# Performance work log

Measured on AMD Instinct MI355X. Metric: run time of the kernel, lower is better.

The kernel has to match this reference:

```python
import jax, jax.numpy as jnp
import numpy as np


def _binomial_blur(k, C):
    a = np.array([1.0, 2.0, 1.0]) if k == 3 else np.ones(k)
    f = a[:, None] * a[None, :]
    f = f / f.sum()
    # HWIO depthwise kernel: (k, k, 1, C)
    return jnp.asarray(np.broadcast_to(f[:, :, None, None], (k, k, 1, C)).copy(), jnp.float32)


def setup_inputs() -> dict:
    key = jax.random.key(0)
    x = jax.random.normal(key, (32, 64, 64, 128), dtype=jnp.float32)
    blur_kernel = _binomial_blur(3, 128)  # fixed (non-learned) binomial low-pass filter
    return {"x": x, "blur_kernel": blur_kernel}


def reference(x, blur_kernel):
    B, T, F, C = x.shape
    # 1) 2x2 max pool, stride 1, SAME (pool_mode='max')
    p = jax.lax.reduce_window(x, -jnp.inf, jax.lax.max,
                              (1, 2, 2, 1), (1, 1, 1, 1), 'SAME')
    # 2) depthwise antialiasing blur, 3x3, SAME
    b = jax.lax.conv_general_dilated(
        p, blur_kernel, window_strides=(1, 1), padding='SAME',
        dimension_numbers=('NHWC', 'HWIO', 'NHWC'), feature_group_count=C)
    # 3) polyphase decomposition (stride 2). Order matches permute_polyphase:
    #    p0=(even,even), p1=(odd,even), p2=(even,odd), p3=(odd,odd)
    cands = jnp.stack([b[:, 0::2, 0::2], b[:, 1::2, 0::2],
                       b[:, 0::2, 1::2], b[:, 1::2, 1::2]], axis=1)  # [B,4,T/2,F/2,C]
    # 4) l2 criterion: pick candidate with max l2 norm per example
    norms = jnp.sqrt(jnp.sum(cands * cands, axis=(2, 3, 4)))  # [B,4]
    idx = jnp.argmax(norms, axis=1)  # [B]
    # 5) gather selected polyphase component
    out = jnp.take_along_axis(cands, idx[:, None, None, None, None], axis=1)[:, 0]
    return out  # [B, T/2, F/2, C]
```

## Files before the change

kernel.cpp:

```cpp
#include <hip/hip_runtime.h>
#include <hip/hip_bf16.h>
#include <float.h>


#define NEGF (-FLT_MAX)

typedef float vfloat4 __attribute__((ext_vector_type(4)));
typedef unsigned vuint4 __attribute__((ext_vector_type(4)));

__device__ __forceinline__ float4 f4max(float4 a, float4 b) {
    return make_float4(fmaxf(a.x, b.x), fmaxf(a.y, b.y),
                       fmaxf(a.z, b.z), fmaxf(a.w, b.w));
}
__device__ __forceinline__ float4 f4add(float4 a, float4 b) {
    return make_float4(a.x + b.x, a.y + b.y, a.z + b.z, a.w + b.w);
}
__device__ __forceinline__ float4 f4b3(float4 a, float4 b, float4 c) {
    return make_float4(fmaf(2.f, b.x, a.x + c.x), fmaf(2.f, b.y, a.y + c.y),
                       fmaf(2.f, b.z, a.z + c.z), fmaf(2.f, b.w, a.w + c.w));
}
__device__ __forceinline__ float4 Z4() { return make_float4(0.f, 0.f, 0.f, 0.f); }

__device__ __forceinline__ float bf2f(unsigned h) {
    return __uint_as_float(h << 16);
}
__device__ __forceinline__ unsigned pku(float a, float b) {
    union { __hip_bfloat162 h2; unsigned u; } cv;
    cv.h2 = __float22bfloat162_rn(make_float2(a, b));
    return cv.u;
}
__device__ __forceinline__ vuint4 pkpair(float4 a, float4 b, float s) {
    vuint4 r = { pku(a.x * s, a.y * s), pku(a.z * s, a.w * s),
                 pku(b.x * s, b.y * s), pku(b.z * s, b.w * s) };
    return r;
}

__device__ __forceinline__ void load_hm(const float4* __restrict__ xb, int r,
                                        const int voff[7], float4 hm[6]) {
    if (r < 0 || r > 63) {
#pragma unroll
        for (int j = 0; j < 6; ++j) hm[j] = make_float4(NEGF, NEGF, NEGF, NEGF);
        return;
    }
    const float4* row = xb + (size_t)r * (64 * 32);
    float4 xv[7];
#pragma unroll
    for (int j = 0; j < 7; ++j) xv[j] = row[voff[j]];
#pragma unroll
    for (int j = 0; j < 6; ++j) hm[j] = f4max(xv[j], xv[j + 1]);
}

__global__ __launch_bounds__(256, 2) void aps_norm_store_kernel(
        const float* __restrict__ xg, float4* __restrict__ partial4,
        vuint4* __restrict__ cand) {
    int blk = blockIdx.x;
    int c8 = blk & 7, j = blk >> 3;
    int b = ((j >> 4) << 3) | c8;
    int r16 = j & 15;
    int ct = r16 >> 3, h = r16 & 7;

    int tid = threadIdx.x;
    int cg = tid & 31;
    int gc = ct * 8 + (tid >> 5);
    int C = gc * 4;
    int t0 = h * 8;

    const float4* xb = (const float4*)xg + (size_t)b * (64 * 64 * 32);

    int voff[7];
#pragma unroll
    for (int j2 = 0; j2 < 7; ++j2) {
        int c = C - 1 + j2;
        c = c < 0 ? 0 : (c > 63 ? 63 : c);
        voff[j2] = c * 32 + cg;
    }
    bool zp0 = (gc == 0), zp5 = (gc == 15);

    float4 hmP[6];
    load_hm(xb, t0 - 1, voff, hmP);
    float4 xvA[7], xvB[7];
    {
        const float4* rowA = xb + (size_t)t0 * (64 * 32);
        const float4* rowB = xb + (size_t)(t0 + 1) * (64 * 32);
#pragma unroll
        for (int j2 = 0; j2 < 7; ++j2) xvA[j2] = rowA[voff[j2]];
#pragma unroll
        for (int j2 = 0; j2 < 7; ++j2) xvB[j2] = rowB[voff[j2]];
    }

    float4 uM1[4], uM2[4];
#pragma unroll
    for (int j2 = 0; j2 < 4; ++j2) { uM1[j2] = Z4(); uM2[j2] = Z4(); }
    float aEE = 0.f, aEO = 0.f, aOE = 0.f, aOO = 0.f;

#pragma unroll
    for (int i = 0; i < 10; ++i) {
        int pr = t0 - 1 + i;
        int rN = pr + 3; rN = rN > 63 ? 63 : rN;
        const float4* rowN = xb + (size_t)rN * (64 * 32);
        float4 xvN[7];
#pragma unroll
        for (int j2 = 0; j2 < 7; ++j2) xvN[j2] = rowN[voff[j2]];

        bool rv = (pr + 1) <= 63;
        float4 hmN[6];
#pragma unroll
        for (int j2 = 0; j2 < 6; ++j2)
            hmN[j2] = rv ? f4max(xvA[j2], xvA[j2 + 1])
                         : make_float4(NEGF, NEGF, NEGF, NEGF);

        float4 p[6];
#pragma unroll
        for (int j2 = 0; j2 < 6; ++j2) p[j2] = f4max(hmP[j2], hmN[j2]);
        if (zp0) p[0] = Z4();
        if (zp5) p[5] = Z4();
        bool urow = (pr >= 0) & (pr <= 63);
        float4 u[4];
#pragma unroll
        for (int j2 = 0; j2 < 4; ++j2)
            u[j2] = urow ? f4b3(p[j2], p[j2 + 1], p[j2 + 2]) : Z4();

        if (i >= 2) {
            float4 bb[4];
            float sE = 0.f, sO = 0.f;
#pragma unroll
            for (int j2 = 0; j2 < 4; ++j2) {
                bb[j2] = f4b3(uM2[j2], uM1[j2], u[j2]);
                float d = bb[j2].x * bb[j2].x + bb[j2].y * bb[j2].y
                        + bb[j2].z * bb[j2].z + bb[j2].w * bb[j2].w;
                if (j2 & 1) sO += d; else sE += d;
            }
            sE *= (1.f / 256.f); sO *= (1.f / 256.f);
            if ((i & 1) == 0) { aEE += sE; aEO += sO; }
            else              { aOE += sE; aOO += sO; }

            int tp = i & 1;
            int tt = (t0 + i - 2) >> 1;
            size_t base = ((((size_t)tp * 32 + b) * 32 + tt) * 16 + gc) * 64 + cg;
            cand[base]      = pkpair(bb[0], bb[2], 0.0625f);
            cand[base + 32] = pkpair(bb[1], bb[3], 0.0625f);
        }

#pragma unroll
        for (int j2 = 0; j2 < 6; ++j2) hmP[j2] = hmN[j2];
#pragma unroll
        for (int j2 = 0; j2 < 7; ++j2) { xvA[j2] = xvB[j2]; xvB[j2] = xvN[j2]; }
#pragma unroll
        for (int j2 = 0; j2 < 4; ++j2) { uM2[j2] = uM1[j2]; uM1[j2] = u[j2]; }
    }

    __shared__ float4 sm4[256];
    sm4[tid] = make_float4(aEE, aEO, aOE, aOO);
    __syncthreads();
    for (int s = 128; s >= 1; s >>= 1) {
        if (tid < s) sm4[tid] = f4add(sm4[tid], sm4[tid + s]);
        __syncthreads();
    }
    if (tid == 0) partial4[b * 16 + r16] = sm4[0];
}

__global__ __launch_bounds__(256) void aps_copy_kernel(
        const vuint4* __restrict__ cand, const float4* __restrict__ partial4,
        float* __restrict__ outg) {
    __shared__ float4 psm[16];
    __shared__ int ksm;
    int blk = blockIdx.x;
    int c8 = blk & 7, j = blk >> 3;
    int b = ((j >> 6) << 3) | c8;
    int r64 = j & 63;
    int tt = r64 >> 1, gh = r64 & 1;
    int tid = threadIdx.x;

    if (tid < 16) psm[tid] = partial4[b * 16 + tid];
    __syncthreads();
    if (tid == 0) {
        float4 tot = Z4();
        for (int jj = 0; jj < 16; ++jj) tot = f4add(tot, psm[jj]);
        float n0 = tot.x, n1 = tot.z, n2 = tot.y, n3 = tot.w;
        int k = 0; float best = n0;
        if (n1 > best) { best = n1; k = 1; }
        if (n2 > best) { best = n2; k = 2; }
        if (n3 > best) { best = n3; k = 3; }
        ksm = k;
    }
    __syncthreads();
    int k = ksm;
    int tp = k & 1, fp = k >> 1;
    int cg = tid & 31;
    int gc = gh * 8 + (tid >> 5);
    size_t base = ((((size_t)tp * 32 + b) * 32 + tt) * 16 + gc) * 64
                + (size_t)fp * 32 + cg;
    vuint4 v = cand[base];

    size_t obase = (((size_t)b * 32 + tt) * 32) * 32 + cg;
    vfloat4 o0 = { bf2f(v.x & 0xffffu), bf2f(v.x >> 16),
                   bf2f(v.y & 0xffffu), bf2f(v.y >> 16) };
    vfloat4 o1 = { bf2f(v.z & 0xffffu), bf2f(v.z >> 16),
                   bf2f(v.w & 0xffffu), bf2f(v.w >> 16) };
    __builtin_nontemporal_store(o0, (vfloat4*)outg + obase + (size_t)(2 * gc) * 32);
    __builtin_nontemporal_store(o1, (vfloat4*)outg + obase + (size_t)(2 * gc + 1) * 32);
}


__global__ __launch_bounds__(256, 2) void aps_norm_kernel(
        const float* __restrict__ xg, float4* __restrict__ partial4) {
    int blk = blockIdx.x;
    int h = blk & 7, ct = (blk >> 3) & 1, b = blk >> 4;
    int tid = threadIdx.x;
    int cg = tid & 31;
    int gc = ct * 8 + (tid >> 5);
    int C = gc * 4;
    int t0 = h * 8;

    const float4* xb = (const float4*)xg + (size_t)b * (64 * 64 * 32);

    int voff[7];
#pragma unroll
    for (int j = 0; j < 7; ++j) {
        int c = C - 1 + j;
        c = c < 0 ? 0 : (c > 63 ? 63 : c);
        voff[j] = c * 32 + cg;
    }
    bool zp0 = (gc == 0), zp5 = (gc == 15);

    float4 hmP[6];
    load_hm(xb, t0 - 1, voff, hmP);
    float4 uM1[4], uM2[4];
#pragma unroll
    for (int j = 0; j < 4; ++j) { uM1[j] = Z4(); uM2[j] = Z4(); }
    float aEE = 0.f, aEO = 0.f, aOE = 0.f, aOO = 0.f;

#pragma unroll
    for (int i = 0; i < 10; ++i) {
        int pr = t0 - 1 + i;
        float4 hmN[6];
        load_hm(xb, pr + 1, voff, hmN);
        float4 p[6];
#pragma unroll
        for (int j = 0; j < 6; ++j) p[j] = f4max(hmP[j], hmN[j]);
        if (zp0) p[0] = Z4();
        if (zp5) p[5] = Z4();
        bool urow = (pr >= 0) & (pr <= 63);
        float4 u[4];
#pragma unroll
        for (int j = 0; j < 4; ++j)
            u[j] = urow ? f4b3(p[j], p[j + 1], p[j + 2]) : Z4();
#pragma unroll
        for (int j = 0; j < 6; ++j) hmP[j] = hmN[j];
        if (i >= 2) {
            float sE = 0.f, sO = 0.f;
#pragma unroll
            for (int j = 0; j < 4; ++j) {
                float4 bb = f4b3(uM2[j], uM1[j], u[j]);
                float d = bb.x * bb.x + bb.y * bb.y + bb.z * bb.z + bb.w * bb.w;
                if (j & 1) sO += d; else sE += d;
            }
            sE *= (1.f / 256.f); sO *= (1.f / 256.f);
            if ((i & 1) == 0) { aEE += sE; aEO += sO; }
            else              { aOE += sE; aOO += sO; }
        }
#pragma unroll
        for (int j = 0; j < 4; ++j) { uM2[j] = uM1[j]; uM1[j] = u[j]; }
    }

    __shared__ float4 sm4[256];
    sm4[tid] = make_float4(aEE, aEO, aOE, aOO);
    __syncthreads();
    for (int s = 128; s >= 1; s >>= 1) {
        if (tid < s) sm4[tid] = f4add(sm4[tid], sm4[tid + s]);
        __syncthreads();
    }
    if (tid == 0) partial4[blk] = sm4[0];
}

__global__ __launch_bounds__(256, 2) void aps_gather_kernel(
        const float* __restrict__ xg, const float4* __restrict__ partial4,
        float* __restrict__ outg) {
    int blk = blockIdx.x;
    int h = blk & 7, ct = (blk >> 3) & 1, b = blk >> 4;
    int tid = threadIdx.x;
    int cg = tid & 31;
    int gc = ct * 8 + (tid >> 5);
    int C = gc * 4;

    float4 tot = Z4();
    for (int j = 0; j < 16; ++j) tot = f4add(tot, partial4[b * 16 + j]);
    float n0 = tot.x, n1 = tot.z, n2 = tot.y, n3 = tot.w;
    int k = 0; float best = n0;
    if (n1 > best) { best = n1; k = 1; }
    if (n2 > best) { best = n2; k = 2; }
    if (n3 > best) { best = n3; k = 3; }
    int tp = k & 1, fp = k >> 1;

    const float4* xb = (const float4*)xg + (size_t)b * (64 * 64 * 32);
    float4* ob = (float4*)outg + (size_t)b * (32 * 32 * 32);

    int voff[7];
#pragma unroll
    for (int j = 0; j < 7; ++j) {
        int c = C - 1 + j;
        c = c < 0 ? 0 : (c > 63 ? 63 : c);
        voff[j] = c * 32 + cg;
    }
    bool zp0 = (gc == 0), zp5 = (gc == 15);

    int sbase = h * 8 + tp;
    float4 hmP[6];
    load_hm(xb, sbase - 1, voff, hmP);
    float4 uM1[2], uM2[2];
#pragma unroll
    for (int j = 0; j < 2; ++j) { uM1[j] = Z4(); uM2[j] = Z4(); }

#pragma unroll
    for (int i = 0; i < 9; ++i) {
        int pr = sbase - 1 + i;
        float4 hmN[6];
        load_hm(xb, pr + 1, voff, hmN);
        float4 p[6];
#pragma unroll
        for (int j = 0; j < 6; ++j) p[j] = f4max(hmP[j], hmN[j]);
        if (zp0) p[0] = Z4();
        if (zp5) p[5] = Z4();
        bool urow = (pr >= 0) & (pr <= 63);
        float4 u[2];
        if (fp == 0) {
            u[0] = urow ? f4b3(p[0], p[1], p[2]) : Z4();
            u[1] = urow ? f4b3(p[2], p[3], p[4]) : Z4();
        } else {
            u[0] = urow ? f4b3(p[1], p[2], p[3]) : Z4();
            u[1] = urow ? f4b3(p[3], p[4], p[5]) : Z4();
        }
#pragma unroll
        for (int j = 0; j < 6; ++j) hmP[j] = hmN[j];
        if (i >= 2 && (i & 1) == 0) {
            int tt = 4 * h + (i >> 1) - 1;
#pragma unroll
            for (int jj = 0; jj < 2; ++jj) {
                float4 bb = f4b3(uM2[jj], uM1[jj], u[jj]);
                bb.x *= 0.0625f; bb.y *= 0.0625f; bb.z *= 0.0625f; bb.w *= 0.0625f;
                int ff = 2 * gc + jj;
                ob[((size_t)tt * 32 + ff) * 32 + cg] = bb;
            }
        }
#pragma unroll
        for (int j = 0; j < 2; ++j) { uM2[j] = uM1[j]; uM1[j] = u[j]; }
    }
}

extern "C" void kernel_launch(void* const* d_in, const int* in_sizes, int n_in,
                              void* d_out, int out_size, void* d_ws, size_t ws_size,
                              hipStream_t stream) {
    const float* x = (const float*)d_in[0];
    float4* partial4 = (float4*)d_ws;
    const size_t CAND_OFF = 8192;
    const size_t CAND_BYTES = (size_t)4 * 32 * 32 * 32 * 128 * 2;
    float* out = (float*)d_out;

    if (ws_size >= CAND_OFF + CAND_BYTES) {
        vuint4* cand = (vuint4*)((char*)d_ws + CAND_OFF);
        aps_norm_store_kernel<<<512, 256, 0, stream>>>(x, partial4, cand);
        aps_copy_kernel<<<2048, 256, 0, stream>>>(cand, partial4, out);
    } else {
        aps_norm_kernel<<<512, 256, 0, stream>>>(x, partial4);
        aps_gather_kernel<<<512, 256, 0, stream>>>(x, partial4, out);
    }
}
```

Before: 29.73 us.

## Fuse norm and copy kernels via grid-wide atomic barrier, holding candidates in registers

Merges the two-kernel path into one persistent-style kernel. Each block keeps its packed bf16 polyphase candidates in registers and publishes its partial norms. It then waits on a global atomic counter until all 512 blocks finish, and writes the selected phase straight to the output. This drops the bf16 candidate round trip through global memory and one kernel launch, but adds a memset launch and a spin barrier that relies on all 512 blocks being co-resident, plus extra register pressure from the held values.

```diff
diff --git a/kernel.cpp b/kernel.cpp
--- a/kernel.cpp
+++ b/kernel.cpp
@@ -50,9 +50,9 @@
     for (int j = 0; j < 6; ++j) hm[j] = f4max(xv[j], xv[j + 1]);
 }
 
-__global__ __launch_bounds__(256, 2) void aps_norm_store_kernel(
+__global__ __launch_bounds__(256, 2) void aps_fused_kernel(
         const float* __restrict__ xg, float4* __restrict__ partial4,
-        vuint4* __restrict__ cand) {
+        unsigned* __restrict__ counter, float* __restrict__ outg) {
     int blk = blockIdx.x;
     int c8 = blk & 7, j = blk >> 3;
     int b = ((j >> 4) << 3) | c8;
@@ -60,7 +60,7 @@
     int ct = r16 >> 3, h = r16 & 7;
 
     int tid = threadIdx.x;
-    int cg = tid & 31;
+    int cgi = tid & 31;
     int gc = ct * 8 + (tid >> 5);
     int C = gc * 4;
     int t0 = h * 8;
@@ -72,7 +72,7 @@
     for (int j2 = 0; j2 < 7; ++j2) {
         int c = C - 1 + j2;
         c = c < 0 ? 0 : (c > 63 ? 63 : c);
-        voff[j2] = c * 32 + cg;
+        voff[j2] = c * 32 + cgi;
     }
     bool zp0 = (gc == 0), zp5 = (gc == 15);
 
@@ -92,6 +92,7 @@
 #pragma unroll
     for (int j2 = 0; j2 < 4; ++j2) { uM1[j2] = Z4(); uM2[j2] = Z4(); }
     float aEE = 0.f, aEO = 0.f, aOE = 0.f, aOO = 0.f;
+    vuint4 held0[8], held1[8];
 
 #pragma unroll
     for (int i = 0; i < 10; ++i) {
@@ -134,11 +135,8 @@
             if ((i & 1) == 0) { aEE += sE; aEO += sO; }
             else              { aOE += sE; aOO += sO; }
 
-            int tp = i & 1;
-            int tt = (t0 + i - 2) >> 1;
-            size_t base = ((((size_t)tp * 32 + b) * 32 + tt) * 16 + gc) * 64 + cg;
-            cand[base]      = pkpair(bb[0], bb[2], 0.0625f);
-            cand[base + 32] = pkpair(bb[1], bb[3], 0.0625f);
+            held0[i - 2] = pkpair(bb[0], bb[2], 0.0625f);
+            held1[i - 2] = pkpair(bb[1], bb[3], 0.0625f);
         }
 
 #pragma unroll
@@ -156,21 +154,22 @@
         if (tid < s) sm4[tid] = f4add(sm4[tid], sm4[tid + s]);
         __syncthreads();
     }
-    if (tid == 0) partial4[b * 16 + r16] = sm4[0];
-}
-
-__global__ __launch_bounds__(256) void aps_copy_kernel(
-        const vuint4* __restrict__ cand, const float4* __restrict__ partial4,
-        float* __restrict__ outg) {
+
+    if (tid == 0) {
+        partial4[b * 16 + r16] = sm4[0];
+        __threadfence();
+        __hip_atomic_fetch_add(counter, 1u, __ATOMIC_RELEASE,
+                               __HIP_MEMORY_SCOPE_AGENT);
+        while (__hip_atomic_load(counter, __ATOMIC_ACQUIRE,
+                                 __HIP_MEMORY_SCOPE_AGENT) < 512u) {
+            __builtin_amdgcn_s_sleep(2);
+        }
+        __threadfence();
+    }
+    __syncthreads();
+
     __shared__ float4 psm[16];
     __shared__ int ksm;
-    int blk = blockIdx.x;
-    int c8 = blk & 7, j = blk >> 3;
-    int b = ((j >> 6) << 3) | c8;
-    int r64 = j & 63;
-    int tt = r64 >> 1, gh = r64 & 1;
-    int tid = threadIdx.x;
-
     if (tid < 16) psm[tid] = partial4[b * 16 + tid];
     __syncthreads();
     if (tid == 0) {
@@ -186,19 +185,22 @@
     __syncthreads();
     int k = ksm;
     int tp = k & 1, fp = k >> 1;
-    int cg = tid & 31;
-    int gc = gh * 8 + (tid >> 5);
-    size_t base = ((((size_t)tp * 32 + b) * 32 + tt) * 16 + gc) * 64
-                + (size_t)fp * 32 + cg;
-    vuint4 v = cand[base];
-
-    size_t obase = (((size_t)b * 32 + tt) * 32) * 32 + cg;
-    vfloat4 o0 = { bf2f(v.x & 0xffffu), bf2f(v.x >> 16),
-                   bf2f(v.y & 0xffffu), bf2f(v.y >> 16) };
-    vfloat4 o1 = { bf2f(v.z & 0xffffu), bf2f(v.z >> 16),
-                   bf2f(v.w & 0xffffu), bf2f(v.w >> 16) };
-    __builtin_nontemporal_store(o0, (vfloat4*)outg + obase + (size_t)(2 * gc) * 32);
-    __builtin_nontemporal_store(o1, (vfloat4*)outg + obase + (size_t)(2 * gc + 1) * 32);
+
+#pragma unroll
+    for (int e2 = 0; e2 < 4; ++e2) {
+        vuint4 v0, v1;
+        if (tp == 0) { v0 = held0[2 * e2];     v1 = held1[2 * e2]; }
+        else         { v0 = held0[2 * e2 + 1]; v1 = held1[2 * e2 + 1]; }
+        vuint4 v = fp ? v1 : v0;
+        int tt = 4 * h + e2;
+        size_t obase = (((size_t)b * 32 + tt) * 32) * 32 + cgi;
+        vfloat4 o0 = { bf2f(v.x & 0xffffu), bf2f(v.x >> 16),
+                       bf2f(v.y & 0xffffu), bf2f(v.y >> 16) };
+        vfloat4 o1 = { bf2f(v.z & 0xffffu), bf2f(v.z >> 16),
+                       bf2f(v.w & 0xffffu), bf2f(v.w >> 16) };
+        __builtin_nontemporal_store(o0, (vfloat4*)outg + obase + (size_t)(2 * gc) * 32);
+        __builtin_nontemporal_store(o1, (vfloat4*)outg + obase + (size_t)(2 * gc + 1) * 32);
+    }
 }
 
 
@@ -352,14 +354,12 @@
                               hipStream_t stream) {
     const float* x = (const float*)d_in[0];
     float4* partial4 = (float4*)d_ws;
-    const size_t CAND_OFF = 8192;
-    const size_t CAND_BYTES = (size_t)4 * 32 * 32 * 32 * 128 * 2;
+    unsigned* counter = (unsigned*)((char*)d_ws + 8192);
     float* out = (float*)d_out;
 
-    if (ws_size >= CAND_OFF + CAND_BYTES) {
-        vuint4* cand = (vuint4*)((char*)d_ws + CAND_OFF);
-        aps_norm_store_kernel<<<512, 256, 0, stream>>>(x, partial4, cand);
-        aps_copy_kernel<<<2048, 256, 0, stream>>>(cand, partial4, out);
+    if (ws_size >= 8192 + sizeof(unsigned)) {
+        hipMemsetAsync(counter, 0, sizeof(unsigned), stream);
+        aps_fused_kernel<<<512, 256, 0, stream>>>(x, partial4, counter, out);
     } else {
         aps_norm_kernel<<<512, 256, 0, stream>>>(x, partial4);
         aps_gather_kernel<<<512, 256, 0, stream>>>(x, partial4, out);
```

Result: slower. 98.13 us (+230.0%).
